# Optimization experiments

Hardware: AMD Instinct MI355X
Metric: run time of the kernel (lower is better)

The kernel has to match this reference:

```python
import jax, jax.numpy as jnp
import numpy as np

B, W, D = 8, 1024, 1024
HEADS, KDIM, VDIM = 16, 64, 64


def setup_inputs() -> dict:
    key = jax.random.key(0)
    k1, k2, k3, k4 = jax.random.split(key, 4)
    # he_normal-ish scaling for weights
    s = (2.0 / D) ** 0.5
    return {
        "inputs": jax.random.normal(k1, (B, W, D), dtype=jnp.float32),
        "Wq": jax.random.normal(k2, (D, HEADS * KDIM), dtype=jnp.float32) * s,
        "Wk": jax.random.normal(k3, (D, HEADS * KDIM), dtype=jnp.float32) * s,
        "Wv": jax.random.normal(k4, (D, HEADS * VDIM), dtype=jnp.float32) * s,
    }


def reference(inputs, Wq, Wk, Wv):
    # Self-attention: memory = inputs
    bsz, win, _ = inputs.shape
    # DenseHeads: linear projection, reshaped to (B, W, heads, head_units)
    q = (inputs @ Wq).reshape(bsz, win, HEADS, KDIM)
    k = (inputs @ Wk).reshape(bsz, win, HEADS, KDIM)
    v = (inputs @ Wv).reshape(bsz, win, HEADS, VDIM)
    scale = KDIM ** (-0.5)
    # scores[b,q,h,m] = sum_k Q[b,q,h,k] * K[b,m,h,k]
    scores = jnp.einsum("bqhk,bmhk->bqhm", q, k) * scale
    attn = jax.nn.softmax(scores, axis=-1)
    # out[b,q,h,v] = sum_m attn[b,q,h,m] * V[b,m,h,v]
    out = jnp.einsum("bqhm,bmhv->bqhv", attn, v)
    return out
```

## Files before the change

kernel.cpp:

```cpp
#include <hip/hip_runtime.h>
#include <stdint.h>


using bf16x8 = __attribute__((ext_vector_type(8))) __bf16;
using f32x4  = __attribute__((ext_vector_type(4))) float;
using f16x4  = __attribute__((ext_vector_type(4))) _Float16;

union frag_u  { uint4 u4; bf16x8 f; };
union vfrag_u { uint2 u2; f16x4 f; };
union pfrag_u { unsigned int u[2]; f16x4 f; };

__device__ inline unsigned short f2bf(float x){
  unsigned int u = __float_as_uint(x);
  u += 0x7fffu + ((u >> 16) & 1u);
  return (unsigned short)(u >> 16);
}

__device__ inline unsigned int pkrtz_u32(float a, float b){
  auto r = __builtin_amdgcn_cvt_pkrtz(a, b);
  unsigned int u; __builtin_memcpy(&u, &r, 4); return u;
}

__device__ inline void gl_lds16(const void* g, void* l){
  __builtin_amdgcn_global_load_lds(
      (const __attribute__((address_space(1))) void*)g,
      (__attribute__((address_space(3))) void*)l, 16, 0, 0);
}

__global__ void cast_all(const float* __restrict__ X,
                         const float* __restrict__ Wq, const float* __restrict__ Wk,
                         const float* __restrict__ Wv,
                         unsigned short* __restrict__ Xb,
                         unsigned short* __restrict__ Wt){
  __shared__ float tile[64][65];
  int bid = blockIdx.x;
  if (bid < 8192){
    int i = (bid * 256 + threadIdx.x) * 4;
    float4 v = *(const float4*)(X + i);
    ushort4 o;
    o.x = f2bf(v.x); o.y = f2bf(v.y); o.z = f2bf(v.z); o.w = f2bf(v.w);
    *(ushort4*)(Xb + i) = o;
    return;
  }
  int id = bid - 8192;
  int proj = id >> 8;
  int rem  = id & 255;
  int kt = rem & 15, nt = rem >> 4;
  const float* Wsrc = (proj == 0) ? Wq : ((proj == 1) ? Wk : Wv);
  int k0 = kt * 64, n0 = nt * 64;
  int tx = threadIdx.x & 63, ty = threadIdx.x >> 6;
  for (int i = 0; i < 16; i++){
    int k = i * 4 + ty;
    tile[k][tx] = Wsrc[(k0 + k) * 1024 + n0 + tx];
  }
  __syncthreads();
  for (int i = 0; i < 16; i++){
    int n = i * 4 + ty;
    Wt[(proj * 1024 + n0 + n) * 1024 + k0 + tx] = f2bf(tile[tx][n]);
  }
}

__global__ void gemm_qkv(const unsigned short* __restrict__ Xb,
                         const unsigned short* __restrict__ Wt,
                         unsigned short* __restrict__ QK,
                         unsigned short* __restrict__ Vt){
  __shared__ __align__(16) unsigned short Abuf[128 * 64];
  __shared__ __align__(16) unsigned short Bbuf[128 * 64];
  int bid = blockIdx.x;
  int bx = bid % 24, by = bid / 24;
  int w = threadIdx.x >> 6, lane = threadIdx.x & 63;
  int g = lane >> 4, li = lane & 15;
  int lrow = lane >> 3, lcol = lane & 7;
  int wm = (w >> 1) * 64, wn = (w & 1) * 64;
  f32x4 acc[4][4] = {};

  for (int k0 = 0; k0 < 1024; k0 += 64){
    __syncthreads();
    for (int i = 0; i < 4; i++){
      int idx = w * 4 + i;
      int row = idx * 8 + lrow;
      gl_lds16(Xb + (by * 128 + row) * 1024 + k0 + lcol * 8, Abuf + idx * 512);
      gl_lds16(Wt + (bx * 128 + row) * 1024 + k0 + lcol * 8, Bbuf + idx * 512);
    }
    __syncthreads();
    for (int c = 0; c < 2; c++){
      frag_u a[4], b[4];
      for (int i = 0; i < 4; i++)
        a[i].u4 = *(const uint4*)(Abuf + (wm + i * 16 + li) * 64 + c * 32 + g * 8);
      for (int j = 0; j < 4; j++)
        b[j].u4 = *(const uint4*)(Bbuf + (wn + j * 16 + li) * 64 + c * 32 + g * 8);
      for (int i = 0; i < 4; i++)
        for (int j = 0; j < 4; j++)
          acc[i][j] = __builtin_amdgcn_mfma_f32_16x16x32_bf16(a[i].f, b[j].f, acc[i][j], 0, 0, 0);
    }
  }
  if (bx >= 16){
    for (int i = 0; i < 4; i++){
      int row = by * 128 + wm + i * 16 + g * 4;
      int bb = row >> 10, m = row & 1023;
      for (int j = 0; j < 4; j++){
        int vc = bx * 128 + wn + j * 16 + li - 2048;
        int hh = vc >> 6, dd = vc & 63;
        uint2 cv;
        cv.x = pkrtz_u32(acc[i][j][0], acc[i][j][1]);
        cv.y = pkrtz_u32(acc[i][j][2], acc[i][j][3]);
        *(uint2*)(Vt + ((size_t)(bb * 16 + hh) * 64 + dd) * 1024 + m) = cv;
      }
    }
  } else {
    float sc = (bx < 8) ? 0.1803368801111f : 1.0f;
    for (int i = 0; i < 4; i++){
      int row = by * 128 + wm + i * 16 + g * 4;
      for (int j = 0; j < 4; j++){
        int col = bx * 128 + wn + j * 16 + li;
        for (int r = 0; r < 4; r++)
          QK[(size_t)(row + r) * 2048 + col] = f2bf(acc[i][j][r] * sc);
      }
    }
  }
}

__global__ __launch_bounds__(256) void attn(const unsigned short* __restrict__ QK,
                                            const unsigned short* __restrict__ Vt,
                                            float* __restrict__ Out){
  __shared__ __align__(16) unsigned short Kbuf[2][64 * 64];
  __shared__ __align__(16) unsigned short Vbuf[2][64 * 64];
  int id = blockIdx.x;
  int bh = id & 127, qb = id >> 7;
  int b = bh >> 4, h = bh & 15;
  int w = threadIdx.x >> 6, lane = threadIdx.x & 63;
  int g = lane >> 4, li = lane & 15;
  int lrow = lane >> 3, lcol = lane & 7;
  int scol = ((lcol ^ lrow) & 7) * 8;

  const unsigned short* Kg = QK + (size_t)b * 1024 * 2048 + 1024 + h * 64;
  const unsigned short* Vg = Vt + (size_t)bh * 65536;

  int idx0 = w * 2, row0 = idx0 * 8 + lrow;
  int idx1 = w * 2 + 1, row1 = idx1 * 8 + lrow;

  auto stage = [&](int mt, int p){
    int m0 = mt * 64;
    gl_lds16(Kg + (size_t)(m0 + row0) * 2048 + scol, &Kbuf[p][idx0 * 512]);
    gl_lds16(Vg + row0 * 1024 + m0 + scol,           &Vbuf[p][idx0 * 512]);
    gl_lds16(Kg + (size_t)(m0 + row1) * 2048 + scol, &Kbuf[p][idx1 * 512]);
    gl_lds16(Vg + row1 * 1024 + m0 + scol,           &Vbuf[p][idx1 * 512]);
  };

  frag_u qf[2][2];
  for (int u = 0; u < 2; u++){
    int tok = b * 1024 + qb * 128 + w * 32 + u * 16 + li;
    const unsigned short* qp = QK + (size_t)tok * 2048 + h * 64 + g * 8;
    qf[u][0].u4 = *(const uint4*)(qp);
    qf[u][1].u4 = *(const uint4*)(qp + 32);
  }

  f32x4 o[2][4] = {};
  float psum[2] = {0.f, 0.f};
  const f32x4 bias = {-10.f, -10.f, -10.f, -10.f};

  stage(0, 0);

  for (int mt = 0; mt < 16; mt++){
    int p = mt & 1;
    asm volatile("s_barrier" ::: "memory");
    if (mt < 15){
      stage(mt + 1, p ^ 1);
      asm volatile("s_waitcnt vmcnt(4)" ::: "memory");
    } else {
      asm volatile("s_waitcnt vmcnt(0)" ::: "memory");
    }
    asm volatile("s_barrier" ::: "memory");

    f32x4 s[2][4];
    for (int u = 0; u < 2; u++)
      for (int t = 0; t < 4; t++)
        s[u][t] = bias;
    for (int t = 0; t < 4; t++){
      for (int c = 0; c < 2; c++){
        frag_u kf;
        kf.u4 = *(const uint4*)(&Kbuf[p][(t * 16 + li) * 64 + ((((c << 2) + g) ^ (li & 7)) << 3)]);
        s[0][t] = __builtin_amdgcn_mfma_f32_16x16x32_bf16(kf.f, qf[0][c].f, s[0][t], 0, 0, 0);
        s[1][t] = __builtin_amdgcn_mfma_f32_16x16x32_bf16(kf.f, qf[1][c].f, s[1][t], 0, 0, 0);
      }
    }

    pfrag_u pf[2][4];
    for (int u = 0; u < 2; u++){
      for (int t = 0; t < 4; t++){
        float p0 = __builtin_exp2f(s[u][t][0]);
        float p1 = __builtin_exp2f(s[u][t][1]);
        float p2 = __builtin_exp2f(s[u][t][2]);
        float p3 = __builtin_exp2f(s[u][t][3]);
        psum[u] += (p0 + p1) + (p2 + p3);
        pf[u][t].u[0] = pkrtz_u32(p0, p1);
        pf[u][t].u[1] = pkrtz_u32(p2, p3);
      }
    }

    for (int tv = 0; tv < 4; tv++){
      for (int t = 0; t < 4; t++){
        int gg = ((t * 2 + (g >> 1)) ^ (li & 7));
        vfrag_u vf;
        vf.u2 = *(const uint2*)(&Vbuf[p][(tv * 16 + li) * 64 + gg * 8 + (g & 1) * 4]);
        o[0][tv] = __builtin_amdgcn_mfma_f32_16x16x16f16(vf.f, pf[0][t].f, o[0][tv], 0, 0, 0);
        o[1][tv] = __builtin_amdgcn_mfma_f32_16x16x16f16(vf.f, pf[1][t].f, o[1][tv], 0, 0, 0);
      }
    }
  }

  for (int u = 0; u < 2; u++){
    psum[u] += __shfl_xor(psum[u], 16);
    psum[u] += __shfl_xor(psum[u], 32);
  }

  for (int u = 0; u < 2; u++){
    float inv = 1.f / psum[u];
    int tok = b * 1024 + qb * 128 + w * 32 + u * 16 + li;
    float* op = Out + (size_t)tok * 1024 + h * 64 + g * 4;
    for (int tv = 0; tv < 4; tv++){
      float4 v4;
      v4.x = o[u][tv][0] * inv; v4.y = o[u][tv][1] * inv;
      v4.z = o[u][tv][2] * inv; v4.w = o[u][tv][3] * inv;
      *(float4*)(op + tv * 16) = v4;
    }
  }
}

extern "C" void kernel_launch(void* const* d_in, const int* in_sizes, int n_in,
                              void* d_out, int out_size, void* d_ws, size_t ws_size,
                              hipStream_t stream) {
  const float* X  = (const float*)d_in[0];
  const float* Wq = (const float*)d_in[1];
  const float* Wk = (const float*)d_in[2];
  const float* Wv = (const float*)d_in[3];
  float* Out = (float*)d_out;
  char* ws = (char*)d_ws;
  unsigned short* Xb = (unsigned short*)(ws);
  unsigned short* Wt = (unsigned short*)(ws + (size_t)16 * 1024 * 1024);
  unsigned short* QK = (unsigned short*)(ws + (size_t)22 * 1024 * 1024);
  unsigned short* Vt = (unsigned short*)(ws + (size_t)54 * 1024 * 1024);

  cast_all<<<8960, 256, 0, stream>>>(X, Wq, Wk, Wv, Xb, Wt);
  gemm_qkv<<<1536, 256, 0, stream>>>(Xb, Wt, QK, Vt);
  attn    <<<1024, 256, 0, stream>>>(QK, Vt, Out);
}
```

Baseline: 221.6 us.

## Load K and V fragments directly from global memory, dropping LDS staging

The attention kernel no longer stages K and V tiles through double-buffered shared memory with barriers. Each wave now loads its MFMA fragments straight from global memory into registers, relying on cache hits because the four waves in a block read the same K/V tiles. This removes the barriers and LDS traffic, but it gives up the explicit prefetch overlap and issues four times as many global loads per block, some of them narrow uint2 strided loads.

```diff
diff --git a/kernel.cpp b/kernel.cpp
--- a/kernel.cpp
+++ b/kernel.cpp
@@ -123,29 +123,11 @@
 __global__ __launch_bounds__(256) void attn(const unsigned short* __restrict__ QK,
                                             const unsigned short* __restrict__ Vt,
                                             float* __restrict__ Out){
-  __shared__ __align__(16) unsigned short Kbuf[2][64 * 64];
-  __shared__ __align__(16) unsigned short Vbuf[2][64 * 64];
   int id = blockIdx.x;
   int bh = id & 127, qb = id >> 7;
   int b = bh >> 4, h = bh & 15;
   int w = threadIdx.x >> 6, lane = threadIdx.x & 63;
   int g = lane >> 4, li = lane & 15;
-  int lrow = lane >> 3, lcol = lane & 7;
-  int scol = ((lcol ^ lrow) & 7) * 8;
-
-  const unsigned short* Kg = QK + (size_t)b * 1024 * 2048 + 1024 + h * 64;
-  const unsigned short* Vg = Vt + (size_t)bh * 65536;
-
-  int idx0 = w * 2, row0 = idx0 * 8 + lrow;
-  int idx1 = w * 2 + 1, row1 = idx1 * 8 + lrow;
-
-  auto stage = [&](int mt, int p){
-    int m0 = mt * 64;
-    gl_lds16(Kg + (size_t)(m0 + row0) * 2048 + scol, &Kbuf[p][idx0 * 512]);
-    gl_lds16(Vg + row0 * 1024 + m0 + scol,           &Vbuf[p][idx0 * 512]);
-    gl_lds16(Kg + (size_t)(m0 + row1) * 2048 + scol, &Kbuf[p][idx1 * 512]);
-    gl_lds16(Vg + row1 * 1024 + m0 + scol,           &Vbuf[p][idx1 * 512]);
-  };
 
   frag_u qf[2][2];
   for (int u = 0; u < 2; u++){
@@ -159,31 +141,32 @@
   float psum[2] = {0.f, 0.f};
   const f32x4 bias = {-10.f, -10.f, -10.f, -10.f};
 
-  stage(0, 0);
+  const unsigned short* Kp = QK + (size_t)b * 1024 * 2048 + 1024 + h * 64
+                           + (size_t)li * 2048 + g * 8;
+  const unsigned short* Vp = Vt + (size_t)bh * 65536 + (size_t)li * 1024 + g * 4;
 
   for (int mt = 0; mt < 16; mt++){
-    int p = mt & 1;
-    asm volatile("s_barrier" ::: "memory");
-    if (mt < 15){
-      stage(mt + 1, p ^ 1);
-      asm volatile("s_waitcnt vmcnt(4)" ::: "memory");
-    } else {
-      asm volatile("s_waitcnt vmcnt(0)" ::: "memory");
-    }
-    asm volatile("s_barrier" ::: "memory");
+    int m0 = mt * 64;
 
     f32x4 s[2][4];
+    frag_u kf[4][2];
+    for (int t = 0; t < 4; t++)
+      for (int c = 0; c < 2; c++)
+        kf[t][c].u4 = *(const uint4*)(Kp + (size_t)(m0 + t * 16) * 2048 + c * 32);
     for (int u = 0; u < 2; u++)
       for (int t = 0; t < 4; t++)
         s[u][t] = bias;
     for (int t = 0; t < 4; t++){
       for (int c = 0; c < 2; c++){
-        frag_u kf;
-        kf.u4 = *(const uint4*)(&Kbuf[p][(t * 16 + li) * 64 + ((((c << 2) + g) ^ (li & 7)) << 3)]);
-        s[0][t] = __builtin_amdgcn_mfma_f32_16x16x32_bf16(kf.f, qf[0][c].f, s[0][t], 0, 0, 0);
-        s[1][t] = __builtin_amdgcn_mfma_f32_16x16x32_bf16(kf.f, qf[1][c].f, s[1][t], 0, 0, 0);
-      }
-    }
+        s[0][t] = __builtin_amdgcn_mfma_f32_16x16x32_bf16(kf[t][c].f, qf[0][c].f, s[0][t], 0, 0, 0);
+        s[1][t] = __builtin_amdgcn_mfma_f32_16x16x32_bf16(kf[t][c].f, qf[1][c].f, s[1][t], 0, 0, 0);
+      }
+    }
+
+    vfrag_u vf[4][4];
+    for (int tv = 0; tv < 4; tv++)
+      for (int t = 0; t < 4; t++)
+        vf[tv][t].u2 = *(const uint2*)(Vp + (size_t)tv * 16 * 1024 + m0 + t * 16);
 
     pfrag_u pf[2][4];
     for (int u = 0; u < 2; u++){
@@ -200,11 +183,8 @@
 
     for (int tv = 0; tv < 4; tv++){
       for (int t = 0; t < 4; t++){
-        int gg = ((t * 2 + (g >> 1)) ^ (li & 7));
-        vfrag_u vf;
-        vf.u2 = *(const uint2*)(&Vbuf[p][(tv * 16 + li) * 64 + gg * 8 + (g & 1) * 4]);
-        o[0][tv] = __builtin_amdgcn_mfma_f32_16x16x16f16(vf.f, pf[0][t].f, o[0][tv], 0, 0, 0);
-        o[1][tv] = __builtin_amdgcn_mfma_f32_16x16x16f16(vf.f, pf[1][t].f, o[1][tv], 0, 0, 0);
+        o[0][tv] = __builtin_amdgcn_mfma_f32_16x16x16f16(vf[tv][t].f, pf[0][t].f, o[0][tv], 0, 0, 0);
+        o[1][tv] = __builtin_amdgcn_mfma_f32_16x16x16f16(vf[tv][t].f, pf[1][t].f, o[1][tv], 0, 0, 0);
       }
     }
   }
```

Measured after the change: 328.8 us. 1.48x slower.
